# Kernel optimization log

Measured on AMD Instinct MI355X. Metric: run time of the kernel, lower is better.

Reference implementation:

```python
import jax, jax.numpy as jnp
import numpy as np
import math

SUB_LEN = 5

def _row_mask(index, sub_len, win_len):
    # Faithful port of logsparseAttention.row_mask (numpy, built at trace time).
    log_l = math.ceil(math.log2(sub_len))
    mask = np.zeros(win_len, dtype=np.float32)
    if (win_len // sub_len) * 2 * log_l > index:
        mask[: index + 1] = 1.0
    else:
        while index >= 0:
            if index - log_l + 1 < 0:
                mask[:index] = 1.0
                break
            mask[index - log_l + 1 : index + 1] = 1.0
            for i in range(log_l):
                new_index = index - log_l + 1 - 2 ** i
                if index - new_index <= sub_len and new_index >= 0:
                    mask[new_index] = 1.0
            index -= sub_len
    return mask

def _log_mask(win_len, sub_len):
    m = np.stack([_row_mask(i, sub_len, win_len) for i in range(win_len)])
    return m[None, None]  # [1, 1, L, L]

def setup_inputs() -> dict:
    key = jax.random.key(0)
    kq, kk, kv = jax.random.split(key, 3)
    B, L, H, D = 4, 2048, 16, 64
    return {
        "queries": jax.random.normal(kq, (B, L, H, D), dtype=jnp.float32),
        "keys": jax.random.normal(kk, (B, L, H, D), dtype=jnp.float32),
        "values": jax.random.normal(kv, (B, L, H, D), dtype=jnp.float32),
        "attn_mask": jnp.zeros((1,), dtype=jnp.int32),  # unused by the module
    }

def reference(queries, keys, values, attn_mask):
    L = queries.shape[1]
    mask = jnp.asarray(_log_mask(L, SUB_LEN), dtype=queries.dtype)  # [1,1,L,L]
    q = jnp.swapaxes(queries, 1, 2)            # [B, H, L, D]
    k = jnp.transpose(keys, (0, 2, 3, 1))      # [B, H, D, L]
    v = jnp.swapaxes(values, 1, 2)             # [B, H, L, D]
    pre_att = jnp.matmul(q, k)                 # [B, H, L, L] (no scaling: scale=None)
    pre_att = pre_att * mask + (-1e9) * (1.0 - mask)
    att = jax.nn.softmax(pre_att, axis=-1)
    return jnp.matmul(att, v)                  # [B, H, L, D]
```

## Files before the change

kernel.cpp:

```cpp
#include <hip/hip_runtime.h>


typedef __attribute__((ext_vector_type(8))) short short8;
typedef __attribute__((ext_vector_type(4))) float floatx4;
typedef _Float16 half8 __attribute__((ext_vector_type(8)));
typedef _Float16 half4 __attribute__((ext_vector_type(4)));

#define NB 4
#define NL 2048
#define NH 16
#define ND 64
#define PADK 72
#define PADQ 72

static __device__ __forceinline__ unsigned short f2bf(float f) {
    unsigned int u = __float_as_uint(f);
    u += 0x7fff + ((u >> 16) & 1);
    return (unsigned short)(u >> 16);
}
static __device__ __forceinline__ float bf2f(unsigned short h) {
    return __uint_as_float(((unsigned int)h) << 16);
}

__global__ __launch_bounds__(256)
void conv_kv(const float* __restrict__ Kg, const float* __restrict__ Vg,
             _Float16* __restrict__ Kf, _Float16* __restrict__ Vt) {
    __shared__ float tile[64][65];
    const int kt = blockIdx.x;
    const int bh = blockIdx.y;
    const int b  = bh >> 4, h = bh & 15;
    const int t  = threadIdx.x;
    const int row = t >> 2;
    const int seg = (t & 3) * 16;
    const size_t gsrc = (((size_t)(b * NL + kt * 64 + row) * NH + h) << 6) + seg;
    {
        float kv[16];
        #pragma unroll
        for (int i = 0; i < 16; i += 4) *(float4*)(kv + i) = *(const float4*)(Kg + gsrc + i);
        half8 o0, o1;
        #pragma unroll
        for (int j2 = 0; j2 < 8; ++j2) { o0[j2] = (_Float16)kv[j2]; o1[j2] = (_Float16)kv[8 + j2]; }
        _Float16* kd = Kf + (((size_t)(bh * NL + kt * 64 + row)) << 6) + seg;
        *(half8*)kd = o0;
        *(half8*)(kd + 8) = o1;
    }
    {
        #pragma unroll
        for (int i = 0; i < 16; i += 4) {
            float4 v = *(const float4*)(Vg + gsrc + i);
            tile[row][seg + i + 0] = v.x;
            tile[row][seg + i + 1] = v.y;
            tile[row][seg + i + 2] = v.z;
            tile[row][seg + i + 3] = v.w;
        }
    }
    __syncthreads();
    #pragma unroll
    for (int pass = 0; pass < 2; ++pass) {
        const int d  = pass * 32 + (t >> 3);
        const int kk = (t & 7) * 8;
        half8 o;
        #pragma unroll
        for (int j2 = 0; j2 < 8; ++j2) o[j2] = (_Float16)tile[kk + j2][d];
        *(half8*)(Vt + (((size_t)(bh * 64 + d)) << 11) + kt * 64 + kk) = o;
    }
}

__global__ __launch_bounds__(512, 4)
void lsattn_main(const float* __restrict__ Qg,
                 const _Float16* __restrict__ Kf,
                 const _Float16* __restrict__ Vt,
                 float* __restrict__ Og) {
    __shared__ alignas(16) _Float16 Ks[64 * PADK];
    __shared__ alignas(16) _Float16 Vs[64 * PADK];
    __shared__ alignas(16) _Float16 Ps[8 * 16 * PADQ];

    const int id   = (int)blockIdx.x;
    const int bh   = id & 63;
    const int pr   = id >> 6;
    const int tid  = threadIdx.x;
    const int lane = tid & 63;
    const int w    = tid >> 6;
    const int col  = lane & 15;
    const int quad = lane >> 4;

    const int sa   = (w < 4) ? pr : (31 - pr);
    const int qrow = sa * 64 + (w & 3) * 16 + col;

    half8 qf[2];
    {
        const float* qp = Qg + (((size_t)((bh >> 4) * NL + qrow) * NH + (bh & 15)) << 6) + quad * 8;
        #pragma unroll
        for (int c = 0; c < 2; ++c) {
            float4 a = *(const float4*)(qp + c * 32);
            float4 b = *(const float4*)(qp + c * 32 + 4);
            qf[c][0] = (_Float16)a.x; qf[c][1] = (_Float16)a.y;
            qf[c][2] = (_Float16)a.z; qf[c][3] = (_Float16)a.w;
            qf[c][4] = (_Float16)b.x; qf[c][5] = (_Float16)b.y;
            qf[c][6] = (_Float16)b.z; qf[c][7] = (_Float16)b.w;
        }
    }

    floatx4 ofrag[4];
    #pragma unroll
    for (int i = 0; i < 4; ++i) ofrag[i] = floatx4{0.f, 0.f, 0.f, 0.f};
    float m_run = -1e30f, l_run = 0.f;

    const int srow = tid >> 3;
    const int sseg = (tid & 7) * 8;
    const _Float16* kgb = Kf + (((size_t)(bh * NL)) << 6) + (srow << 6) + sseg;
    const _Float16* vgb = Vt + (((size_t)bh) << 17) + ((size_t)srow << 11) + sseg;
    _Float16* pbuf = Ps + w * 16 * PADQ;

    const int TB = 31 - pr;

    half8 kpre = *(const half8*)(kgb);
    half8 vpre = *(const half8*)(vgb);

    for (int t = 0; t <= TB; ++t) {
        const int j0 = t * 64;
        __syncthreads();
        *(half8*)(Ks + srow * PADK + sseg) = kpre;
        *(half8*)(Vs + srow * PADK + sseg) = vpre;
        if (t < TB) {
            kpre = *(const half8*)(kgb + (t + 1) * 4096);
            vpre = *(const half8*)(vgb + (t + 1) * 64);
        }
        __syncthreads();

        if (t > sa) continue;

        floatx4 stf[4];
        #pragma unroll
        for (int f = 0; f < 4; ++f) {
            floatx4 acc = floatx4{0.f, 0.f, 0.f, 0.f};
            #pragma unroll
            for (int c = 0; c < 2; ++c) {
                half8 kfr = *(const half8*)(Ks + (f * 16 + col) * PADK + c * 32 + quad * 8);
                acc = __builtin_amdgcn_mfma_f32_16x16x32_f16(kfr, qf[c], acc, 0, 0, 0);
            }
            stf[f] = acc;
        }

        if (t == sa) {
            #pragma unroll
            for (int f = 0; f < 4; ++f)
                #pragma unroll
                for (int r = 0; r < 4; ++r) {
                    const int key = j0 + f * 16 + quad * 4 + r;
                    if (key > qrow) stf[f][r] = -1e30f;
                }
        }

        float mt = -1e30f;
        #pragma unroll
        for (int f = 0; f < 4; ++f)
            #pragma unroll
            for (int r = 0; r < 4; ++r) mt = fmaxf(mt, stf[f][r]);
        mt = fmaxf(mt, __shfl_xor(mt, 16));
        mt = fmaxf(mt, __shfl_xor(mt, 32));
        const float m_new = fmaxf(m_run, mt);
        const float alpha = __expf(m_run - m_new);
        float ls = 0.f;
        #pragma unroll
        for (int f = 0; f < 4; ++f)
            #pragma unroll
            for (int r = 0; r < 4; ++r) {
                const float p = __expf(stf[f][r] - m_new);
                stf[f][r] = p;
                ls += p;
            }
        ls += __shfl_xor(ls, 16);
        ls += __shfl_xor(ls, 32);
        l_run = l_run * alpha + ls;
        m_run = m_new;
        #pragma unroll
        for (int mc = 0; mc < 4; ++mc) ofrag[mc] *= alpha;

        #pragma unroll
        for (int f = 0; f < 4; ++f) {
            half4 hp;
            hp[0] = (_Float16)stf[f][0]; hp[1] = (_Float16)stf[f][1];
            hp[2] = (_Float16)stf[f][2]; hp[3] = (_Float16)stf[f][3];
            *(half4*)(pbuf + col * PADQ + f * 16 + quad * 4) = hp;
        }
        half8 pf0 = *(const half8*)(pbuf + col * PADQ + quad * 8);
        half8 pf1 = *(const half8*)(pbuf + col * PADQ + 32 + quad * 8);

        #pragma unroll
        for (int mc = 0; mc < 4; ++mc) {
            half8 vf0 = *(const half8*)(Vs + (mc * 16 + col) * PADK + quad * 8);
            half8 vf1 = *(const half8*)(Vs + (mc * 16 + col) * PADK + 32 + quad * 8);
            ofrag[mc] = __builtin_amdgcn_mfma_f32_16x16x32_f16(vf0, pf0, ofrag[mc], 0, 0, 0);
            ofrag[mc] = __builtin_amdgcn_mfma_f32_16x16x32_f16(vf1, pf1, ofrag[mc], 0, 0, 0);
        }
    }

    const float inv = 1.f / l_run;
    float* op = Og + ((size_t)bh * NL + qrow) * ND;
    #pragma unroll
    for (int mc = 0; mc < 4; ++mc) {
        float4 o;
        o.x = ofrag[mc][0] * inv;
        o.y = ofrag[mc][1] * inv;
        o.z = ofrag[mc][2] * inv;
        o.w = ofrag[mc][3] * inv;
        *(float4*)(op + mc * 16 + quad * 4) = o;
    }
}

__global__ __launch_bounds__(256)
void lsattn_fb(const float* __restrict__ Qg,
               const float* __restrict__ Kg,
               const float* __restrict__ Vg,
               float* __restrict__ Og) {
    __shared__ alignas(16) unsigned short Kh[64 * PADK];
    __shared__ alignas(16) unsigned short Kl[64 * PADK];
    __shared__ alignas(16) unsigned short Vh[64 * PADK];

    const int qt   = 31 - (int)blockIdx.x;
    const int bh   = blockIdx.y;
    const int tid  = threadIdx.x;
    const int lane = tid & 63;
    const int w    = tid >> 6;
    const int col  = lane & 15;
    const int quad = lane >> 4;
    const int qrow = qt * 64 + w * 16 + col;

    short8 qhi[2], qlo[2];
    {
        const float* qp = Qg + ((bh >> 4) * NL + qrow) * (NH * ND) + (bh & 15) * ND + quad * 8;
        #pragma unroll
        for (int c = 0; c < 2; ++c) {
            float qv[8];
            *(float4*)(qv + 0) = *(const float4*)(qp + c * 32);
            *(float4*)(qv + 4) = *(const float4*)(qp + c * 32 + 4);
            #pragma unroll
            for (int j = 0; j < 8; ++j) {
                unsigned short h = f2bf(qv[j]);
                qhi[c][j] = (short)h;
                qlo[c][j] = (short)f2bf(qv[j] - bf2f(h));
            }
        }
    }
    floatx4 ofrag[4];
    #pragma unroll
    for (int i = 0; i < 4; ++i) ofrag[i] = floatx4{0.f, 0.f, 0.f, 0.f};
    float m_run = -1e30f, l_run = 0.f;
    const int skey  = tid >> 2;
    const int sdb   = (tid & 3) * 16;
    const int gbase = (bh >> 4) * NL * NH * ND + (bh & 15) * ND;

    for (int t = 0; t <= qt; ++t) {
        const int j0 = t * 64;
        __syncthreads();
        {
            const int gro = gbase + (j0 + skey) * (NH * ND) + sdb;
            float kv[16], vv[16];
            #pragma unroll
            for (int i = 0; i < 16; i += 4) {
                *(float4*)(kv + i) = *(const float4*)(Kg + gro + i);
                *(float4*)(vv + i) = *(const float4*)(Vg + gro + i);
            }
            short8 h0, h1, l0, l1;
            #pragma unroll
            for (int j = 0; j < 8; ++j) {
                unsigned short h = f2bf(kv[j]);
                h0[j] = (short)h; l0[j] = (short)f2bf(kv[j] - bf2f(h));
                unsigned short g = f2bf(kv[8 + j]);
                h1[j] = (short)g; l1[j] = (short)f2bf(kv[8 + j] - bf2f(g));
            }
            *(short8*)(Kh + skey * PADK + sdb)     = h0;
            *(short8*)(Kh + skey * PADK + sdb + 8) = h1;
            *(short8*)(Kl + skey * PADK + sdb)     = l0;
            *(short8*)(Kl + skey * PADK + sdb + 8) = l1;
            #pragma unroll
            for (int i = 0; i < 16; ++i) Vh[(sdb + i) * PADK + skey] = f2bf(vv[i]);
        }
        __syncthreads();

        floatx4 stf[4];
        #pragma unroll
        for (int f = 0; f < 4; ++f) {
            floatx4 acc = floatx4{0.f, 0.f, 0.f, 0.f};
            #pragma unroll
            for (int c = 0; c < 2; ++c) {
                short8 kh = *(const short8*)(Kh + (f * 16 + col) * PADK + c * 32 + quad * 8);
                short8 kl = *(const short8*)(Kl + (f * 16 + col) * PADK + c * 32 + quad * 8);
                acc = __builtin_amdgcn_mfma_f32_16x16x32_bf16(kh, qhi[c], acc, 0, 0, 0);
                acc = __builtin_amdgcn_mfma_f32_16x16x32_bf16(kl, qhi[c], acc, 0, 0, 0);
                acc = __builtin_amdgcn_mfma_f32_16x16x32_bf16(kh, qlo[c], acc, 0, 0, 0);
            }
            stf[f] = acc;
        }
        if (t == qt) {
            #pragma unroll
            for (int f = 0; f < 4; ++f)
                #pragma unroll
                for (int r = 0; r < 4; ++r) {
                    const int key = j0 + f * 16 + quad * 4 + r;
                    if (key > qrow) stf[f][r] = -1e30f;
                }
        }
        float mt = -1e30f;
        #pragma unroll
        for (int f = 0; f < 4; ++f)
            #pragma unroll
            for (int r = 0; r < 4; ++r) mt = fmaxf(mt, stf[f][r]);
        mt = fmaxf(mt, __shfl_xor(mt, 16));
        mt = fmaxf(mt, __shfl_xor(mt, 32));
        const float m_new = fmaxf(m_run, mt);
        const float alpha = __expf(m_run - m_new);
        float ls = 0.f;
        #pragma unroll
        for (int f = 0; f < 4; ++f)
            #pragma unroll
            for (int r = 0; r < 4; ++r) {
                const float p = __expf(stf[f][r] - m_new);
                stf[f][r] = p; ls += p;
            }
        ls += __shfl_xor(ls, 16);
        ls += __shfl_xor(ls, 32);
        l_run = l_run * alpha + ls;
        m_run = m_new;
        #pragma unroll
        for (int mc = 0; mc < 4; ++mc) ofrag[mc] *= alpha;

        short8 pfrag[2];
        #pragma unroll
        for (int kc = 0; kc < 2; ++kc) {
            #pragma unroll
            for (int jj = 0; jj < 8; ++jj) {
                const int r  = jj & 3;
                const int sq = (quad & 1) * 2 + (jj >> 2);
                const int sl = col + (sq << 4);
                const float va = __shfl(stf[kc * 2 + 0][r], sl);
                const float vb = __shfl(stf[kc * 2 + 1][r], sl);
                pfrag[kc][jj] = (short)f2bf((quad & 2) ? vb : va);
            }
        }
        #pragma unroll
        for (int mc = 0; mc < 4; ++mc) {
            #pragma unroll
            for (int kc = 0; kc < 2; ++kc) {
                short8 vf = *(const short8*)(Vh + (mc * 16 + col) * PADK + kc * 32 + quad * 8);
                ofrag[mc] = __builtin_amdgcn_mfma_f32_16x16x32_bf16(vf, pfrag[kc], ofrag[mc], 0, 0, 0);
            }
        }
    }
    const float inv = 1.f / l_run;
    float* op = Og + ((size_t)bh * NL + qrow) * ND;
    #pragma unroll
    for (int mc = 0; mc < 4; ++mc) {
        float4 o;
        o.x = ofrag[mc][0] * inv; o.y = ofrag[mc][1] * inv;
        o.z = ofrag[mc][2] * inv; o.w = ofrag[mc][3] * inv;
        *(float4*)(op + mc * 16 + quad * 4) = o;
    }
}

extern "C" void kernel_launch(void* const* d_in, const int* in_sizes, int n_in,
                              void* d_out, int out_size, void* d_ws, size_t ws_size,
                              hipStream_t stream) {
    const float* Q = (const float*)d_in[0];
    const float* K = (const float*)d_in[1];
    const float* V = (const float*)d_in[2];
    float* O = (float*)d_out;

    const size_t elems = (size_t)NB * NL * NH * ND;
    if (ws_size >= 2 * elems * sizeof(_Float16)) {
        _Float16* Kf = (_Float16*)d_ws;
        _Float16* Vt = Kf + elems;
        conv_kv<<<dim3(32, 64), dim3(256), 0, stream>>>(K, V, Kf, Vt);
        lsattn_main<<<dim3(1024), dim3(512), 0, stream>>>(Q, Kf, Vt, O);
    } else {
        lsattn_fb<<<dim3(32, 64), dim3(256), 0, stream>>>(Q, K, V, O);
    }
}
```

Baseline: 197.9 us.

## Pair two query row blocks per workgroup, use exp2 softmax with lazy rescale

Each workgroup now handles two 128-row query chunks from opposite ends of the causal range. Every wave keeps fragments for both chunks, so each staged K/V tile in LDS is reused by two query sets, and the grid is halved. The softmax moves to base-2 exponentials, with log2(e) folded into K during the conversion pass. The running-max rescale of the output accumulators is skipped unless the new max exceeds the old one by more than 8. This cuts global-to-LDS traffic, barriers and exp/rescale work per query row, at the cost of roughly double accumulator register pressure and fewer workgroups to spread across the CUs.

Measured after the change: 209.3 us. 5.8% more time.

```diff
diff --git a/kernel.cpp b/kernel.cpp
--- a/kernel.cpp
+++ b/kernel.cpp
@@ -12,6 +12,7 @@
 #define ND 64
 #define PADK 72
 #define PADQ 72
+#define LOG2E 1.44269504088896340736f
 
 static __device__ __forceinline__ unsigned short f2bf(float f) {
     unsigned int u = __float_as_uint(f);
@@ -39,7 +40,10 @@
         for (int i = 0; i < 16; i += 4) *(float4*)(kv + i) = *(const float4*)(Kg + gsrc + i);
         half8 o0, o1;
         #pragma unroll
-        for (int j2 = 0; j2 < 8; ++j2) { o0[j2] = (_Float16)kv[j2]; o1[j2] = (_Float16)kv[8 + j2]; }
+        for (int j2 = 0; j2 < 8; ++j2) {
+            o0[j2] = (_Float16)(kv[j2] * LOG2E);
+            o1[j2] = (_Float16)(kv[8 + j2] * LOG2E);
+        }
         _Float16* kd = Kf + (((size_t)(bh * NL + kt * 64 + row)) << 6) + seg;
         *(half8*)kd = o0;
         *(half8*)(kd + 8) = o1;
@@ -64,6 +68,51 @@
         for (int j2 = 0; j2 < 8; ++j2) o[j2] = (_Float16)tile[kk + j2][d];
         *(half8*)(Vt + (((size_t)(bh * 64 + d)) << 11) + kt * 64 + kk) = o;
     }
+}
+
+static __device__ __forceinline__ void softmax_half(
+    floatx4* s, bool domask, int j0, int qrow, int col, int quad,
+    float& m_run, float& l_run, floatx4* of,
+    _Float16* pbuf, half8& pf0, half8& pf1)
+{
+    if (domask) {
+        #pragma unroll
+        for (int f = 0; f < 4; ++f)
+            #pragma unroll
+            for (int r = 0; r < 4; ++r)
+                if (j0 + f * 16 + quad * 4 + r > qrow) s[f][r] = -1e30f;
+    }
+    float mt = fmaxf(fmaxf(s[0][0], s[0][1]), fmaxf(s[0][2], s[0][3]));
+    #pragma unroll
+    for (int f = 1; f < 4; ++f)
+        mt = fmaxf(mt, fmaxf(fmaxf(s[f][0], s[f][1]), fmaxf(s[f][2], s[f][3])));
+    mt = fmaxf(mt, __shfl_xor(mt, 16));
+    mt = fmaxf(mt, __shfl_xor(mt, 32));
+    if (__any(mt > m_run + 8.f)) {
+        const float mn = fmaxf(m_run, mt);
+        const float al = __builtin_amdgcn_exp2f(m_run - mn);
+        #pragma unroll
+        for (int mc = 0; mc < 4; ++mc) of[mc] *= al;
+        l_run *= al;
+        m_run = mn;
+    }
+    float ls = 0.f;
+    #pragma unroll
+    for (int f = 0; f < 4; ++f) {
+        half4 hp;
+        #pragma unroll
+        for (int r = 0; r < 4; ++r) {
+            const float p = __builtin_amdgcn_exp2f(s[f][r] - m_run);
+            ls += p;
+            hp[r] = (_Float16)p;
+        }
+        *(half4*)(pbuf + col * PADQ + f * 16 + quad * 4) = hp;
+    }
+    ls += __shfl_xor(ls, 16);
+    ls += __shfl_xor(ls, 32);
+    l_run += ls;
+    pf0 = *(const half8*)(pbuf + col * PADQ + quad * 8);
+    pf1 = *(const half8*)(pbuf + col * PADQ + 32 + quad * 8);
 }
 
 __global__ __launch_bounds__(512, 4)
@@ -77,42 +126,53 @@
 
     const int id   = (int)blockIdx.x;
     const int bh   = id & 63;
-    const int pr   = id >> 6;
+    const int j    = id >> 6;
+    const int pp   = (j < 4) ? j : 11 - j;
     const int tid  = threadIdx.x;
     const int lane = tid & 63;
     const int w    = tid >> 6;
     const int col  = lane & 15;
     const int quad = lane >> 4;
-
-    const int sa   = (w < 4) ? pr : (31 - pr);
-    const int qrow = sa * 64 + (w & 3) * 16 + col;
-
-    half8 qf[2];
-    {
-        const float* qp = Qg + (((size_t)((bh >> 4) * NL + qrow) * NH + (bh & 15)) << 6) + quad * 8;
+    const int wq   = w >> 2;
+
+    const int qrowA  = pp * 128 + w * 16 + col;
+    const int qrowB  = (15 - pp) * 128 + w * 16 + col;
+    const int boundA = 2 * pp + wq;
+    const int boundB = 30 - 2 * pp + wq;
+    const int TB     = 31 - 2 * pp;
+
+    half8 qfA[2], qfB[2];
+    {
+        const int b = bh >> 4, h = bh & 15;
+        const float* qpA = Qg + (((size_t)(b * NL + qrowA) * NH + h) << 6) + quad * 8;
+        const float* qpB = Qg + (((size_t)(b * NL + qrowB) * NH + h) << 6) + quad * 8;
         #pragma unroll
         for (int c = 0; c < 2; ++c) {
-            float4 a = *(const float4*)(qp + c * 32);
-            float4 b = *(const float4*)(qp + c * 32 + 4);
-            qf[c][0] = (_Float16)a.x; qf[c][1] = (_Float16)a.y;
-            qf[c][2] = (_Float16)a.z; qf[c][3] = (_Float16)a.w;
-            qf[c][4] = (_Float16)b.x; qf[c][5] = (_Float16)b.y;
-            qf[c][6] = (_Float16)b.z; qf[c][7] = (_Float16)b.w;
-        }
-    }
-
-    floatx4 ofrag[4];
-    #pragma unroll
-    for (int i = 0; i < 4; ++i) ofrag[i] = floatx4{0.f, 0.f, 0.f, 0.f};
-    float m_run = -1e30f, l_run = 0.f;
+            float4 a0 = *(const float4*)(qpA + c * 32);
+            float4 a1 = *(const float4*)(qpA + c * 32 + 4);
+            qfA[c][0] = (_Float16)a0.x; qfA[c][1] = (_Float16)a0.y;
+            qfA[c][2] = (_Float16)a0.z; qfA[c][3] = (_Float16)a0.w;
+            qfA[c][4] = (_Float16)a1.x; qfA[c][5] = (_Float16)a1.y;
+            qfA[c][6] = (_Float16)a1.z; qfA[c][7] = (_Float16)a1.w;
+            float4 b0 = *(const float4*)(qpB + c * 32);
+            float4 b1 = *(const float4*)(qpB + c * 32 + 4);
+            qfB[c][0] = (_Float16)b0.x; qfB[c][1] = (_Float16)b0.y;
+            qfB[c][2] = (_Float16)b0.z; qfB[c][3] = (_Float16)b0.w;
+            qfB[c][4] = (_Float16)b1.x; qfB[c][5] = (_Float16)b1.y;
+            qfB[c][6] = (_Float16)b1.z; qfB[c][7] = (_Float16)b1.w;
+        }
+    }
+
+    floatx4 oA[4], oB[4];
+    #pragma unroll
+    for (int i = 0; i < 4; ++i) { oA[i] = floatx4{0.f,0.f,0.f,0.f}; oB[i] = floatx4{0.f,0.f,0.f,0.f}; }
+    float mA = -1e30f, lA = 0.f, mB = -1e30f, lB = 0.f;
 
     const int srow = tid >> 3;
     const int sseg = (tid & 7) * 8;
     const _Float16* kgb = Kf + (((size_t)(bh * NL)) << 6) + (srow << 6) + sseg;
     const _Float16* vgb = Vt + (((size_t)bh) << 17) + ((size_t)srow << 11) + sseg;
     _Float16* pbuf = Ps + w * 16 * PADQ;
-
-    const int TB = 31 - pr;
 
     half8 kpre = *(const half8*)(kgb);
     half8 vpre = *(const half8*)(vgb);
@@ -128,84 +188,71 @@
         }
         __syncthreads();
 
-        if (t > sa) continue;
-
-        floatx4 stf[4];
-        #pragma unroll
-        for (int f = 0; f < 4; ++f) {
-            floatx4 acc = floatx4{0.f, 0.f, 0.f, 0.f};
-            #pragma unroll
-            for (int c = 0; c < 2; ++c) {
-                half8 kfr = *(const half8*)(Ks + (f * 16 + col) * PADK + c * 32 + quad * 8);
-                acc = __builtin_amdgcn_mfma_f32_16x16x32_f16(kfr, qf[c], acc, 0, 0, 0);
-            }
-            stf[f] = acc;
-        }
-
-        if (t == sa) {
-            #pragma unroll
-            for (int f = 0; f < 4; ++f)
-                #pragma unroll
-                for (int r = 0; r < 4; ++r) {
-                    const int key = j0 + f * 16 + quad * 4 + r;
-                    if (key > qrow) stf[f][r] = -1e30f;
+        const bool actA = (t <= boundA);
+        const bool actB = (t <= boundB);
+        if (actA || actB) {
+            floatx4 sA[4], sB[4];
+            #pragma unroll
+            for (int f = 0; f < 4; ++f) {
+                const _Float16* kr = Ks + (f * 16 + col) * PADK + quad * 8;
+                const half8 k0 = *(const half8*)(kr);
+                const half8 k1 = *(const half8*)(kr + 32);
+                if (actA) {
+                    floatx4 a = floatx4{0.f,0.f,0.f,0.f};
+                    a = __builtin_amdgcn_mfma_f32_16x16x32_f16(k0, qfA[0], a, 0, 0, 0);
+                    a = __builtin_amdgcn_mfma_f32_16x16x32_f16(k1, qfA[1], a, 0, 0, 0);
+                    sA[f] = a;
                 }
-        }
-
-        float mt = -1e30f;
-        #pragma unroll
-        for (int f = 0; f < 4; ++f)
-            #pragma unroll
-            for (int r = 0; r < 4; ++r) mt = fmaxf(mt, stf[f][r]);
-        mt = fmaxf(mt, __shfl_xor(mt, 16));
-        mt = fmaxf(mt, __shfl_xor(mt, 32));
-        const float m_new = fmaxf(m_run, mt);
-        const float alpha = __expf(m_run - m_new);
-        float ls = 0.f;
-        #pragma unroll
-        for (int f = 0; f < 4; ++f)
-            #pragma unroll
-            for (int r = 0; r < 4; ++r) {
-                const float p = __expf(stf[f][r] - m_new);
-                stf[f][r] = p;
-                ls += p;
-            }
-        ls += __shfl_xor(ls, 16);
-        ls += __shfl_xor(ls, 32);
-        l_run = l_run * alpha + ls;
-        m_run = m_new;
-        #pragma unroll
-        for (int mc = 0; mc < 4; ++mc) ofrag[mc] *= alpha;
-
-        #pragma unroll
-        for (int f = 0; f < 4; ++f) {
-            half4 hp;
-            hp[0] = (_Float16)stf[f][0]; hp[1] = (_Float16)stf[f][1];
-            hp[2] = (_Float16)stf[f][2]; hp[3] = (_Float16)stf[f][3];
-            *(half4*)(pbuf + col * PADQ + f * 16 + quad * 4) = hp;
-        }
-        half8 pf0 = *(const half8*)(pbuf + col * PADQ + quad * 8);
-        half8 pf1 = *(const half8*)(pbuf + col * PADQ + 32 + quad * 8);
-
+                if (actB) {
+                    floatx4 b = floatx4{0.f,0.f,0.f,0.f};
+                    b = __builtin_amdgcn_mfma_f32_16x16x32_f16(k0, qfB[0], b, 0, 0, 0);
+                    b = __builtin_amdgcn_mfma_f32_16x16x32_f16(k1, qfB[1], b, 0, 0, 0);
+                    sB[f] = b;
+                }
+            }
+
+            half8 pA0, pA1, pB0, pB1;
+            if (actA) softmax_half(sA, t == boundA, j0, qrowA, col, quad, mA, lA, oA, pbuf, pA0, pA1);
+            if (actB) softmax_half(sB, t == boundB, j0, qrowB, col, quad, mB, lB, oB, pbuf, pB0, pB1);
+
+            #pragma unroll
+            for (int mc = 0; mc < 4; ++mc) {
+                const _Float16* vr = Vs + (mc * 16 + col) * PADK + quad * 8;
+                const half8 v0 = *(const half8*)(vr);
+                const half8 v1 = *(const half8*)(vr + 32);
+                if (actA) {
+                    oA[mc] = __builtin_amdgcn_mfma_f32_16x16x32_f16(v0, pA0, oA[mc], 0, 0, 0);
+                    oA[mc] = __builtin_amdgcn_mfma_f32_16x16x32_f16(v1, pA1, oA[mc], 0, 0, 0);
+                }
+                if (actB) {
+                    oB[mc] = __builtin_amdgcn_mfma_f32_16x16x32_f16(v0, pB0, oB[mc], 0, 0, 0);
+                    oB[mc] = __builtin_amdgcn_mfma_f32_16x16x32_f16(v1, pB1, oB[mc], 0, 0, 0);
+                }
+            }
+        }
+    }
+
+    {
+        const float inv = 1.f / lA;
+        float* op = Og + ((size_t)bh * NL + qrowA) * ND;
         #pragma unroll
         for (int mc = 0; mc < 4; ++mc) {
-            half8 vf0 = *(const half8*)(Vs + (mc * 16 + col) * PADK + quad * 8);
-            half8 vf1 = *(const half8*)(Vs + (mc * 16 + col) * PADK + 32 + quad * 8);
-            ofrag[mc] = __builtin_amdgcn_mfma_f32_16x16x32_f16(vf0, pf0, ofrag[mc], 0, 0, 0);
-            ofrag[mc] = __builtin_amdgcn_mfma_f32_16x16x32_f16(vf1, pf1, ofrag[mc], 0, 0, 0);
-        }
-    }
-
-    const float inv = 1.f / l_run;
-    float* op = Og + ((size_t)bh * NL + qrow) * ND;
-    #pragma unroll
-    for (int mc = 0; mc < 4; ++mc) {
-        float4 o;
-        o.x = ofrag[mc][0] * inv;
-        o.y = ofrag[mc][1] * inv;
-        o.z = ofrag[mc][2] * inv;
-        o.w = ofrag[mc][3] * inv;
-        *(float4*)(op + mc * 16 + quad * 4) = o;
+            float4 o;
+            o.x = oA[mc][0] * inv; o.y = oA[mc][1] * inv;
+            o.z = oA[mc][2] * inv; o.w = oA[mc][3] * inv;
+            *(float4*)(op + mc * 16 + quad * 4) = o;
+        }
+    }
+    {
+        const float inv = 1.f / lB;
+        float* op = Og + ((size_t)bh * NL + qrowB) * ND;
+        #pragma unroll
+        for (int mc = 0; mc < 4; ++mc) {
+            float4 o;
+            o.x = oB[mc][0] * inv; o.y = oB[mc][1] * inv;
+            o.z = oB[mc][2] * inv; o.w = oB[mc][3] * inv;
+            *(float4*)(op + mc * 16 + quad * 4) = o;
+        }
     }
 }
 
@@ -372,7 +419,7 @@
         _Float16* Kf = (_Float16*)d_ws;
         _Float16* Vt = Kf + elems;
         conv_kv<<<dim3(32, 64), dim3(256), 0, stream>>>(K, V, Kf, Vt);
-        lsattn_main<<<dim3(1024), dim3(512), 0, stream>>>(Q, Kf, Vt, O);
+        lsattn_main<<<dim3(512), dim3(512), 0, stream>>>(Q, Kf, Vt, O);
     } else {
         lsattn_fb<<<dim3(32, 64), dim3(256), 0, stream>>>(Q, K, V, O);
     }
```

## Switch attention to 32x32 MFMA tiles with swizzled LDS and exp2 softmax

Applied to the files above, without the earlier changes.

Rewrites the main attention kernel to use 32x32x16 MFMA tiles with 4 waves per block (each wave owning 32 query rows) instead of 16x16x32 tiles with 8 waves. K and V shared tiles use an XOR swizzle instead of padding, and log2(e) is folded into K during conversion so softmax can use exp2. Rescaling of the running max is now lazy, applied only when the max grows by more than a threshold, and the masked upper half of the diagonal tile is skipped. The intent is fewer MFMA and LDS instructions and less softmax overhead, at the cost of higher register pressure and fewer waves per block.

Result: faster. 187.6 us (-5.2%).

```diff
diff --git a/kernel.cpp b/kernel.cpp
--- a/kernel.cpp
+++ b/kernel.cpp
@@ -3,6 +3,7 @@
 
 typedef __attribute__((ext_vector_type(8))) short short8;
 typedef __attribute__((ext_vector_type(4))) float floatx4;
+typedef __attribute__((ext_vector_type(16))) float floatx16;
 typedef _Float16 half8 __attribute__((ext_vector_type(8)));
 typedef _Float16 half4 __attribute__((ext_vector_type(4)));
 
@@ -11,7 +12,9 @@
 #define NH 16
 #define ND 64
 #define PADK 72
-#define PADQ 72
+#define LOG2E 1.44269504088896340736f
+
+#define KSW(row, col8) (((row) << 6) + ((col8) ^ (((row) & 7) << 3)))
 
 static __device__ __forceinline__ unsigned short f2bf(float f) {
     unsigned int u = __float_as_uint(f);
@@ -20,6 +23,12 @@
 }
 static __device__ __forceinline__ float bf2f(unsigned short h) {
     return __uint_as_float(((unsigned int)h) << 16);
+}
+static __device__ __forceinline__ floatx16 fzero16() {
+    floatx16 z;
+    #pragma unroll
+    for (int i = 0; i < 16; ++i) z[i] = 0.f;
+    return z;
 }
 
 __global__ __launch_bounds__(256)
@@ -39,7 +48,10 @@
         for (int i = 0; i < 16; i += 4) *(float4*)(kv + i) = *(const float4*)(Kg + gsrc + i);
         half8 o0, o1;
         #pragma unroll
-        for (int j2 = 0; j2 < 8; ++j2) { o0[j2] = (_Float16)kv[j2]; o1[j2] = (_Float16)kv[8 + j2]; }
+        for (int j2 = 0; j2 < 8; ++j2) {
+            o0[j2] = (_Float16)(kv[j2] * LOG2E);
+            o1[j2] = (_Float16)(kv[8 + j2] * LOG2E);
+        }
         _Float16* kd = Kf + (((size_t)(bh * NL + kt * 64 + row)) << 6) + seg;
         *(half8*)kd = o0;
         *(half8*)(kd + 8) = o1;
@@ -66,14 +78,14 @@
     }
 }
 
-__global__ __launch_bounds__(512, 4)
+__global__ __launch_bounds__(256, 4)
 void lsattn_main(const float* __restrict__ Qg,
                  const _Float16* __restrict__ Kf,
                  const _Float16* __restrict__ Vt,
                  float* __restrict__ Og) {
-    __shared__ alignas(16) _Float16 Ks[64 * PADK];
-    __shared__ alignas(16) _Float16 Vs[64 * PADK];
-    __shared__ alignas(16) _Float16 Ps[8 * 16 * PADQ];
+    __shared__ alignas(16) _Float16 Ks[64 * 64];
+    __shared__ alignas(16) _Float16 Vs[64 * 64];
+    __shared__ alignas(16) _Float16 Ps[4 * 8 * 32 * 8];
 
     const int id   = (int)blockIdx.x;
     const int bh   = id & 63;
@@ -81,19 +93,21 @@
     const int tid  = threadIdx.x;
     const int lane = tid & 63;
     const int w    = tid >> 6;
-    const int col  = lane & 15;
-    const int quad = lane >> 4;
-
-    const int sa   = (w < 4) ? pr : (31 - pr);
-    const int qrow = sa * 64 + (w & 3) * 16 + col;
-
-    half8 qf[2];
+    const int wq   = w & 1;
+    const int lq   = lane & 31;
+    const int hi   = lane >> 5;
+
+    const int sa   = (w < 2) ? pr : 31 - pr;
+    const int qrow = sa * 64 + wq * 32 + lq;
+    const int TB   = 31 - pr;
+
+    half8 qf[4];
     {
-        const float* qp = Qg + (((size_t)((bh >> 4) * NL + qrow) * NH + (bh & 15)) << 6) + quad * 8;
-        #pragma unroll
-        for (int c = 0; c < 2; ++c) {
-            float4 a = *(const float4*)(qp + c * 32);
-            float4 b = *(const float4*)(qp + c * 32 + 4);
+        const float* qp = Qg + (((size_t)((bh >> 4) * NL + qrow) * NH + (bh & 15)) << 6) + hi * 8;
+        #pragma unroll
+        for (int c = 0; c < 4; ++c) {
+            float4 a = *(const float4*)(qp + c * 16);
+            float4 b = *(const float4*)(qp + c * 16 + 4);
             qf[c][0] = (_Float16)a.x; qf[c][1] = (_Float16)a.y;
             qf[c][2] = (_Float16)a.z; qf[c][3] = (_Float16)a.w;
             qf[c][4] = (_Float16)b.x; qf[c][5] = (_Float16)b.y;
@@ -101,111 +115,133 @@
         }
     }
 
-    floatx4 ofrag[4];
-    #pragma unroll
-    for (int i = 0; i < 4; ++i) ofrag[i] = floatx4{0.f, 0.f, 0.f, 0.f};
+    floatx16 o0 = fzero16(), o1 = fzero16();
     float m_run = -1e30f, l_run = 0.f;
 
     const int srow = tid >> 3;
     const int sseg = (tid & 7) * 8;
-    const _Float16* kgb = Kf + (((size_t)(bh * NL)) << 6) + (srow << 6) + sseg;
-    const _Float16* vgb = Vt + (((size_t)bh) << 17) + ((size_t)srow << 11) + sseg;
-    _Float16* pbuf = Ps + w * 16 * PADQ;
-
-    const int TB = 31 - pr;
-
-    half8 kpre = *(const half8*)(kgb);
-    half8 vpre = *(const half8*)(vgb);
+    const _Float16* kgb = Kf + ((size_t)bh * NL + srow) * 64 + sseg;
+    const _Float16* vgb = Vt + ((size_t)bh << 17) + (size_t)srow * NL + sseg;
+    _Float16* pbuf = Ps + w * 2048;
+
+    half8 k0 = *(const half8*)(kgb);
+    half8 k1 = *(const half8*)(kgb + 2048);
+    half8 v0 = *(const half8*)(vgb);
+    half8 v1 = *(const half8*)(vgb + 32 * NL);
 
     for (int t = 0; t <= TB; ++t) {
-        const int j0 = t * 64;
         __syncthreads();
-        *(half8*)(Ks + srow * PADK + sseg) = kpre;
-        *(half8*)(Vs + srow * PADK + sseg) = vpre;
+        *(half8*)(Ks + KSW(srow,      sseg)) = k0;
+        *(half8*)(Ks + KSW(srow + 32, sseg)) = k1;
+        *(half8*)(Vs + KSW(srow,      sseg)) = v0;
+        *(half8*)(Vs + KSW(srow + 32, sseg)) = v1;
         if (t < TB) {
-            kpre = *(const half8*)(kgb + (t + 1) * 4096);
-            vpre = *(const half8*)(vgb + (t + 1) * 64);
+            k0 = *(const half8*)(kgb + (size_t)(t + 1) * 4096);
+            k1 = *(const half8*)(kgb + (size_t)(t + 1) * 4096 + 2048);
+            v0 = *(const half8*)(vgb + (t + 1) * 64);
+            v1 = *(const half8*)(vgb + (t + 1) * 64 + 32 * NL);
         }
         __syncthreads();
 
         if (t > sa) continue;
 
-        floatx4 stf[4];
-        #pragma unroll
-        for (int f = 0; f < 4; ++f) {
-            floatx4 acc = floatx4{0.f, 0.f, 0.f, 0.f};
-            #pragma unroll
-            for (int c = 0; c < 2; ++c) {
-                half8 kfr = *(const half8*)(Ks + (f * 16 + col) * PADK + c * 32 + quad * 8);
-                acc = __builtin_amdgcn_mfma_f32_16x16x32_f16(kfr, qf[c], acc, 0, 0, 0);
-            }
-            stf[f] = acc;
-        }
-
-        if (t == sa) {
-            #pragma unroll
-            for (int f = 0; f < 4; ++f)
+        const bool diag  = (t == sa);
+        const bool skip1 = diag && (wq == 0);
+
+        floatx16 s0 = fzero16(), s1;
+        #pragma unroll
+        for (int c = 0; c < 4; ++c) {
+            half8 kf = *(const half8*)(Ks + KSW(lq, c * 16 + hi * 8));
+            s0 = __builtin_amdgcn_mfma_f32_32x32x16_f16(kf, qf[c], s0, 0, 0, 0);
+        }
+        if (!skip1) {
+            s1 = fzero16();
+            #pragma unroll
+            for (int c = 0; c < 4; ++c) {
+                half8 kf = *(const half8*)(Ks + KSW(32 + lq, c * 16 + hi * 8));
+                s1 = __builtin_amdgcn_mfma_f32_32x32x16_f16(kf, qf[c], s1, 0, 0, 0);
+            }
+        }
+
+        if (diag) {
+            if (wq == 0) {
+                #pragma unroll
+                for (int reg = 0; reg < 16; ++reg) {
+                    const int key = (reg & 3) + ((reg >> 2) << 3) + (hi << 2);
+                    if (key > lq) s0[reg] = -1e30f;
+                }
+            } else {
+                #pragma unroll
+                for (int reg = 0; reg < 16; ++reg) {
+                    const int key = (reg & 3) + ((reg >> 2) << 3) + (hi << 2);
+                    if (key > lq) s1[reg] = -1e30f;
+                }
+            }
+        }
+
+        float mt = s0[0];
+        #pragma unroll
+        for (int reg = 1; reg < 16; ++reg) mt = fmaxf(mt, s0[reg]);
+        if (!skip1) {
+            #pragma unroll
+            for (int reg = 0; reg < 16; ++reg) mt = fmaxf(mt, s1[reg]);
+        }
+        mt = fmaxf(mt, __shfl_xor(mt, 32));
+        if (__any(mt > m_run + 8.f)) {
+            const float mn = fmaxf(m_run, mt);
+            const float al = __builtin_amdgcn_exp2f(m_run - mn);
+            #pragma unroll
+            for (int i = 0; i < 16; ++i) { o0[i] *= al; o1[i] *= al; }
+            l_run *= al;
+            m_run = mn;
+        }
+        float ls = 0.f;
+        #pragma unroll
+        for (int s = 0; s < 4; ++s) {
+            half4 hp;
+            #pragma unroll
+            for (int r = 0; r < 4; ++r) {
+                const float p = __builtin_amdgcn_exp2f(s0[s * 4 + r] - m_run);
+                ls += p; hp[r] = (_Float16)p;
+            }
+            *(half4*)(pbuf + (s * 32 + lq) * 8 + hi * 4) = hp;
+        }
+        if (!skip1) {
+            #pragma unroll
+            for (int s = 0; s < 4; ++s) {
+                half4 hp;
                 #pragma unroll
                 for (int r = 0; r < 4; ++r) {
-                    const int key = j0 + f * 16 + quad * 4 + r;
-                    if (key > qrow) stf[f][r] = -1e30f;
+                    const float p = __builtin_amdgcn_exp2f(s1[s * 4 + r] - m_run);
+                    ls += p; hp[r] = (_Float16)p;
                 }
-        }
-
-        float mt = -1e30f;
-        #pragma unroll
-        for (int f = 0; f < 4; ++f)
-            #pragma unroll
-            for (int r = 0; r < 4; ++r) mt = fmaxf(mt, stf[f][r]);
-        mt = fmaxf(mt, __shfl_xor(mt, 16));
-        mt = fmaxf(mt, __shfl_xor(mt, 32));
-        const float m_new = fmaxf(m_run, mt);
-        const float alpha = __expf(m_run - m_new);
-        float ls = 0.f;
-        #pragma unroll
-        for (int f = 0; f < 4; ++f)
-            #pragma unroll
-            for (int r = 0; r < 4; ++r) {
-                const float p = __expf(stf[f][r] - m_new);
-                stf[f][r] = p;
-                ls += p;
-            }
-        ls += __shfl_xor(ls, 16);
+                *(half4*)(pbuf + ((4 + s) * 32 + lq) * 8 + hi * 4) = hp;
+            }
+        }
         ls += __shfl_xor(ls, 32);
-        l_run = l_run * alpha + ls;
-        m_run = m_new;
-        #pragma unroll
-        for (int mc = 0; mc < 4; ++mc) ofrag[mc] *= alpha;
-
-        #pragma unroll
-        for (int f = 0; f < 4; ++f) {
-            half4 hp;
-            hp[0] = (_Float16)stf[f][0]; hp[1] = (_Float16)stf[f][1];
-            hp[2] = (_Float16)stf[f][2]; hp[3] = (_Float16)stf[f][3];
-            *(half4*)(pbuf + col * PADQ + f * 16 + quad * 4) = hp;
-        }
-        half8 pf0 = *(const half8*)(pbuf + col * PADQ + quad * 8);
-        half8 pf1 = *(const half8*)(pbuf + col * PADQ + 32 + quad * 8);
-
-        #pragma unroll
-        for (int mc = 0; mc < 4; ++mc) {
-            half8 vf0 = *(const half8*)(Vs + (mc * 16 + col) * PADK + quad * 8);
-            half8 vf1 = *(const half8*)(Vs + (mc * 16 + col) * PADK + 32 + quad * 8);
-            ofrag[mc] = __builtin_amdgcn_mfma_f32_16x16x32_f16(vf0, pf0, ofrag[mc], 0, 0, 0);
-            ofrag[mc] = __builtin_amdgcn_mfma_f32_16x16x32_f16(vf1, pf1, ofrag[mc], 0, 0, 0);
+        l_run += ls;
+
+        const int cmax = skip1 ? 2 : 4;
+        for (int c = 0; c < cmax; ++c) {
+            half8 pf  = *(const half8*)(pbuf + ((c * 2 + hi) * 32 + lq) * 8);
+            half8 vf0 = *(const half8*)(Vs + KSW(lq,      c * 16 + hi * 8));
+            half8 vf1 = *(const half8*)(Vs + KSW(32 + lq, c * 16 + hi * 8));
+            o0 = __builtin_amdgcn_mfma_f32_32x32x16_f16(vf0, pf, o0, 0, 0, 0);
+            o1 = __builtin_amdgcn_mfma_f32_32x32x16_f16(vf1, pf, o1, 0, 0, 0);
         }
     }
 
     const float inv = 1.f / l_run;
     float* op = Og + ((size_t)bh * NL + qrow) * ND;
     #pragma unroll
-    for (int mc = 0; mc < 4; ++mc) {
-        float4 o;
-        o.x = ofrag[mc][0] * inv;
-        o.y = ofrag[mc][1] * inv;
-        o.z = ofrag[mc][2] * inv;
-        o.w = ofrag[mc][3] * inv;
-        *(float4*)(op + mc * 16 + quad * 4) = o;
+    for (int s = 0; s < 4; ++s) {
+        float4 x, y;
+        x.x = o0[s * 4 + 0] * inv; x.y = o0[s * 4 + 1] * inv;
+        x.z = o0[s * 4 + 2] * inv; x.w = o0[s * 4 + 3] * inv;
+        *(float4*)(op + s * 8 + hi * 4) = x;
+        y.x = o1[s * 4 + 0] * inv; y.y = o1[s * 4 + 1] * inv;
+        y.z = o1[s * 4 + 2] * inv; y.w = o1[s * 4 + 3] * inv;
+        *(float4*)(op + 32 + s * 8 + hi * 4) = y;
     }
 }
 
@@ -372,7 +408,7 @@
         _Float16* Kf = (_Float16*)d_ws;
         _Float16* Vt = Kf + elems;
         conv_kv<<<dim3(32, 64), dim3(256), 0, stream>>>(K, V, Kf, Vt);
-        lsattn_main<<<dim3(1024), dim3(512), 0, stream>>>(Q, Kf, Vt, O);
+        lsattn_main<<<dim3(1024), dim3(256), 0, stream>>>(Q, Kf, Vt, O);
     } else {
         lsattn_fb<<<dim3(32, 64), dim3(256), 0, stream>>>(Q, K, V, O);
     }
```
